# Kernel optimization log

Measured on AMD Instinct MI355X. Metric: run time of the kernel, lower is better.

Reference implementation:

```python
import jax, jax.numpy as jnp
import numpy as np
from jax import lax

PATCH = 3  # also hist_window since n_history = 1


def setup_inputs() -> dict:
    key = jax.random.key(0)
    k1, k2, k3 = jax.random.split(key, 3)
    B, Seq, F = 128, 3000, 64
    x = jax.random.normal(k1, (B, Seq, F), dtype=jnp.float32)
    agg_w = jax.random.normal(k2, (PATCH, PATCH), dtype=jnp.float32)  # Linear(hist_window=3 -> patch=3)
    agg_b = jax.random.normal(k3, (PATCH,), dtype=jnp.float32)
    return {"x": x, "agg_w": agg_w, "agg_b": agg_b}


def reference(x, agg_w, agg_b):
    # DDI forward with alpha=0.0 (default): for each patch i,
    #   prev   = output[:, i-patch:i, :]            (previous produced patch)
    #   agg    = gelu(Linear(prev.permute(0,2,1))).permute(0,2,1)
    #   output[:, i:i+patch, :] = agg + x[:, i:i+patch, :]
    # Dropout is identity (eval). Strict sequential dep -> lax.scan over chunks.
    B, Seq, F = x.shape
    head = x[:, :PATCH, :]  # first hist_window tokens copied through
    n_chunks = (Seq - PATCH) // PATCH  # 999
    # [n_chunks, B, patch, F]
    chunks = jnp.swapaxes(x[:, PATCH:, :].reshape(B, n_chunks, PATCH, F), 0, 1)

    def step(prev, cur):
        # prev, cur: [B, patch, F]
        # Linear over history axis: out[b,p,f] = sum_h prev[b,h,f] * W[p,h] + b[p]
        agg = jnp.einsum('bhf,ph->bpf', prev, agg_w) + agg_b[None, :, None]
        agg = jax.nn.gelu(agg, approximate=False)  # torch F.gelu default is exact
        res = agg + cur
        return res, res

    _, out_chunks = lax.scan(step, head, chunks)  # [n_chunks, B, patch, F]
    tail = jnp.swapaxes(out_chunks, 0, 1).reshape(B, Seq - PATCH, F)
    return jnp.concatenate([head, tail], axis=1)
```

## Files before the change

kernel.cpp:

```cpp
#include <hip/hip_runtime.h>
#include <math.h>

#define SEQ   3000
#define FDIM  64

#define PPWc  0.23164189f
#define B1f   0.127414796f
#define B2f   (-0.142248368f)
#define B3f   0.7107068705f
#define B4f   (-0.7265760135f)
#define B5f   0.5307027145f
#define NL2Ef (-0.72134752044448170368f)

#define DECL9(p) float p##0,p##1,p##2,p##3,p##4,p##5,p##6,p##7,p##8
#define TOUCH9(P) "+v"(P##0),"+v"(P##1),"+v"(P##2),"+v"(P##3),"+v"(P##4),     \
    "+v"(P##5),"+v"(P##6),"+v"(P##7),"+v"(P##8)

#define PF1S(dst, OFF) asm volatile(                                          \
    "global_load_dword %0, %1, %2 offset:" #OFF                               \
    : "=v"(dst) : "v"(voff), "s"(lbase) : "memory")

#define WAITVM(Nlit, P) do {                                                  \
    asm volatile("s_waitcnt vmcnt(" #Nlit ")" : TOUCH9(P) : : "memory");      \
    __builtin_amdgcn_sched_barrier(0);                                        \
} while (0)

#define ASMA() asm volatile(                                                  \
    "v_fma_f32 %[a], %[wa], %[s], %[q]\n\t"                                   \
    "v_mov_b32_dpp %[d1], %[s] quad_perm:[1,2,0,0] row_mask:0xf bank_mask:0xf\n\t" \
    "v_mov_b32_dpp %[d2], %[s] quad_perm:[2,0,1,1] row_mask:0xf bank_mask:0xf\n\t" \
    "v_fmac_f32 %[a], %[wb], %[d1]\n\t"                                       \
    "v_fmac_f32 %[a], %[wc], %[d2]\n\t"                                       \
    "v_mul_f32 %[u2], %[a], %[a]\n\t"                                         \
    "v_max_f32 %[rl], 0, %[a]\n\t"                                            \
    "v_fma_f32 %[dd], %[ppw], abs(%[a]), 1.0\n\t"                             \
    "v_mul_f32 %[m], %[u2], %[nl2e]\n\t"                                      \
    "v_rcp_f32 %[r], %[dd]\n\t"                                               \
    "v_exp_f32 %[e], %[m]"                                                    \
    : [a]"=&v"(a_), [d1]"=&v"(d1_), [d2]"=&v"(d2_), [u2]"=&v"(u2_),           \
      [dd]"=&v"(dd_), [m]"=&v"(m_), [r]"=&v"(r_), [e]"=&v"(e_), [rl]"=&v"(rl_)\
    : [s]"v"(s), [wa]"v"(wA), [wb]"v"(wB), [wc]"v"(wC), [q]"v"(q),            \
      [ppw]"v"(cPPW), [nl2e]"v"(cNL2E))

#define ASMB(U, OFF) asm volatile(                                            \
    "v_fma_f32 %[c01], %[b2], %[r], %[b1]\n\t"                                \
    "v_fma_f32 %[c23], %[b4], %[r], %[b3]\n\t"                                \
    "v_mul_f32 %[rr], %[r], %[r]\n\t"                                         \
    "v_mul_f32 %[z], -abs(%[a]), %[e]\n\t"                                    \
    "v_add_f32 %[rlu], %[rl], %[u]\n\t"                                       \
    "v_fma_f32 %[pp], %[c23], %[rr], %[c01]\n\t"                              \
    "v_mul_f32 %[r4], %[rr], %[rr]\n\t"                                       \
    "v_mul_f32 %[zr], %[z], %[r]\n\t"                                         \
    "v_fmac_f32 %[pp], %[b5], %[r4]\n\t"                                      \
    "v_fma_f32 %[s], %[pp], %[zr], %[rlu]\n\t"                                \
    "global_store_dword %[vo], %[s], %[ob] offset:" #OFF                      \
    : [s]"=&v"(s), [c01]"=&v"(c01_), [c23]"=&v"(c23_), [rr]"=&v"(rr_),        \
      [r4]"=&v"(r4_), [pp]"=&v"(pp_), [zr]"=&v"(zr_), [z]"=&v"(z_),           \
      [rlu]"=&v"(rlu_)                                                        \
    : [a]"v"(a_), [r]"v"(r_), [e]"v"(e_), [rl]"v"(rl_), [u]"v"(U),            \
      [b1]"v"(cB1), [b2]"v"(cB2), [b3]"v"(cB3), [b4]"v"(cB4), [b5]"v"(cB5),   \
      [vo]"v"(voff), [ob]"s"(obase)                                           \
    : "memory")

#define STEP_LD(U, LD, OFF)  do { ASMA(); PF1S(LD, OFF); ASMB(U, OFF); } while (0)
#define STEP_NOLD(U, OFF)    do { ASMA(); ASMB(U, OFF); } while (0)

#define GRP_LD(P, L) do {                                                     \
    STEP_LD(P##0, L##0, 0); STEP_LD(P##1, L##1, 768); STEP_LD(P##2, L##2, 1536);\
    lbase += 576; obase += 576;                                               \
    STEP_LD(P##3, L##3, 0); STEP_LD(P##4, L##4, 768); STEP_LD(P##5, L##5, 1536);\
    lbase += 576; obase += 576;                                               \
    STEP_LD(P##6, L##6, 0); STEP_LD(P##7, L##7, 768); STEP_LD(P##8, L##8, 1536);\
    lbase += 576; obase += 576;                                               \
} while (0)

#define GRP_NOLD(P) do {                                                      \
    STEP_NOLD(P##0, 0); STEP_NOLD(P##1, 768); STEP_NOLD(P##2, 1536);          \
    obase += 576;                                                             \
    STEP_NOLD(P##3, 0); STEP_NOLD(P##4, 768); STEP_NOLD(P##5, 1536);          \
    obase += 576;                                                             \
    STEP_NOLD(P##6, 0); STEP_NOLD(P##7, 768); STEP_NOLD(P##8, 1536);          \
    obase += 576;                                                             \
} while (0)

#define PF3B(Pa, Pb, Pc) do {                                                 \
    PF1S(Pa, 0); PF1S(Pb, 768); PF1S(Pc, 1536); lbase += 576;                 \
} while (0)
#define PF9B(P) do { PF3B(P##0,P##1,P##2); PF3B(P##3,P##4,P##5);              \
    PF3B(P##6,P##7,P##8); } while (0)

__global__ __launch_bounds__(64, 1) void scan_kernel(
    const float* __restrict__ x,
    const float* __restrict__ w,
    const float* __restrict__ bias,
    float* __restrict__ out)
{
    const int lane = threadIdx.x;
    const int g  = lane >> 2;
    const int pr = lane & 3;
    const int p  = pr < 3 ? pr : 2;

    const int B = blockIdx.x;
    const int xs = B & 7, h = (B >> 3) & 1, j = B >> 4;
    const int i = j * 8 + xs;
    const int b = i >> 1;
    const int fq = ((i & 1) << 1) | h;
    const int f = (fq << 4) + g;

    const int p1i = (p + 1) == 3 ? 0 : p + 1;
    const int p2i = (p + 2) >= 3 ? p - 1 : p + 2;
    float wA = w[p * 3 + p];
    float wB = w[p * 3 + p1i];
    float wC = w[p * 3 + p2i];
    float q  = bias[p];

    float cPPW = PPWc, cNL2E = NL2Ef;
    float cB1 = B1f, cB2 = B2f, cB3 = B3f, cB4 = B4f, cB5 = B5f;

    const int voff = p * 256 + f * 4;
    const float* lbase = x   + (size_t)b * (SEQ * FDIM) + 3 * FDIM;
    float*       obase = out + (size_t)b * (SEQ * FDIM) + 3 * FDIM;
    const float* hbase = x   + (size_t)b * (SEQ * FDIM);
    float*       ohead = out + (size_t)b * (SEQ * FDIM);

    float s = *(const float*)((const char*)hbase + voff);
    asm volatile("" : "+v"(s), "+v"(wA), "+v"(wB), "+v"(wC), "+v"(q),
                      "+v"(cPPW), "+v"(cNL2E), "+v"(cB1), "+v"(cB2),
                      "+v"(cB3), "+v"(cB4), "+v"(cB5));
    asm volatile("global_store_dword %0, %1, %2"
                 :: "v"(voff), "v"(s), "s"(ohead) : "memory");

    float a_, d1_, d2_, u2_, dd_, m_, r_, e_, rl_;
    float c01_, c23_, rr_, r4_, pp_, zr_, z_, rlu_;

    DECL9(LA); DECL9(LB); DECL9(LC); DECL9(LD);

    PF9B(LA);
    PF9B(LB);
    PF9B(LC);
    WAITVM(18, LA);

    #pragma unroll 1
    for (int t = 0; t < 27; ++t) {
        GRP_LD(LA, LD);   WAITVM(27, LB);
        GRP_LD(LB, LA);   WAITVM(27, LC);
        GRP_LD(LC, LB);   WAITVM(27, LD);
        GRP_LD(LD, LC);   WAITVM(27, LA);
    }

    GRP_NOLD(LA);         WAITVM(9, LB);
    GRP_NOLD(LB);         WAITVM(9, LC);
    GRP_NOLD(LC);
}

extern "C" void kernel_launch(void* const* d_in, const int* in_sizes, int n_in,
                              void* d_out, int out_size, void* d_ws, size_t ws_size,
                              hipStream_t stream) {
    const float* x    = (const float*)d_in[0];
    const float* w    = (const float*)d_in[1];
    const float* bias = (const float*)d_in[2];
    float* out        = (float*)d_out;

    hipLaunchKernelGGL(scan_kernel, dim3(512), dim3(64), 0, stream,
                       x, w, bias, out);
}
```

Measured before the change: 61.03 us.

## Process two feature columns per lane with interleaved dual recurrence chains

Each lane now carries two independent scan chains (adjacent features X and Y), interleaving their instructions so one chain's ALU/transcendental latency hides behind the other's. The grid halves from 512 to 256 single-wave blocks, with block-to-(batch,feature) mapping simplified. This adds ILP on the latency-bound serial recurrence at the cost of more registers, half as many wavefronts across the GPU, and a different memory access pattern per block.

Result: slower. 102.9 us (+68.7%).

```diff
diff --git a/kernel.cpp b/kernel.cpp
--- a/kernel.cpp
+++ b/kernel.cpp
@@ -16,78 +16,121 @@
 #define TOUCH9(P) "+v"(P##0),"+v"(P##1),"+v"(P##2),"+v"(P##3),"+v"(P##4),     \
     "+v"(P##5),"+v"(P##6),"+v"(P##7),"+v"(P##8)
 
-#define PF1S(dst, OFF) asm volatile(                                          \
-    "global_load_dword %0, %1, %2 offset:" #OFF                               \
-    : "=v"(dst) : "v"(voff), "s"(lbase) : "memory")
-
-#define WAITVM(Nlit, P) do {                                                  \
-    asm volatile("s_waitcnt vmcnt(" #Nlit ")" : TOUCH9(P) : : "memory");      \
+#define PF2S(dX, dY, OFF) asm volatile(                                       \
+    "global_load_dword %0, %2, %4 offset:" #OFF "\n\t"                        \
+    "global_load_dword %1, %3, %4 offset:" #OFF                               \
+    : "=v"(dX), "=v"(dY) : "v"(voffX), "v"(voffY), "s"(lbase) : "memory")
+
+#define ST2(OFF) asm volatile(                                                \
+    "global_store_dword %0, %2, %4 offset:" #OFF "\n\t"                       \
+    "global_store_dword %1, %3, %4 offset:" #OFF                              \
+    :: "v"(voffX), "v"(voffY), "v"(sx), "v"(sy), "s"(obase) : "memory")
+
+#define WAITVM2(Nlit, PX, PY) do {                                            \
+    asm volatile("s_waitcnt vmcnt(" #Nlit ")"                                 \
+                 : TOUCH9(PX), TOUCH9(PY) : : "memory");                      \
     __builtin_amdgcn_sched_barrier(0);                                        \
 } while (0)
 
-#define ASMA() asm volatile(                                                  \
-    "v_fma_f32 %[a], %[wa], %[s], %[q]\n\t"                                   \
-    "v_mov_b32_dpp %[d1], %[s] quad_perm:[1,2,0,0] row_mask:0xf bank_mask:0xf\n\t" \
-    "v_mov_b32_dpp %[d2], %[s] quad_perm:[2,0,1,1] row_mask:0xf bank_mask:0xf\n\t" \
-    "v_fmac_f32 %[a], %[wb], %[d1]\n\t"                                       \
-    "v_fmac_f32 %[a], %[wc], %[d2]\n\t"                                       \
-    "v_mul_f32 %[u2], %[a], %[a]\n\t"                                         \
-    "v_max_f32 %[rl], 0, %[a]\n\t"                                            \
-    "v_fma_f32 %[dd], %[ppw], abs(%[a]), 1.0\n\t"                             \
-    "v_mul_f32 %[m], %[u2], %[nl2e]\n\t"                                      \
-    "v_rcp_f32 %[r], %[dd]\n\t"                                               \
-    "v_exp_f32 %[e], %[m]"                                                    \
-    : [a]"=&v"(a_), [d1]"=&v"(d1_), [d2]"=&v"(d2_), [u2]"=&v"(u2_),           \
-      [dd]"=&v"(dd_), [m]"=&v"(m_), [r]"=&v"(r_), [e]"=&v"(e_), [rl]"=&v"(rl_)\
-    : [s]"v"(s), [wa]"v"(wA), [wb]"v"(wB), [wc]"v"(wC), [q]"v"(q),            \
-      [ppw]"v"(cPPW), [nl2e]"v"(cNL2E))
-
-#define ASMB(U, OFF) asm volatile(                                            \
-    "v_fma_f32 %[c01], %[b2], %[r], %[b1]\n\t"                                \
-    "v_fma_f32 %[c23], %[b4], %[r], %[b3]\n\t"                                \
-    "v_mul_f32 %[rr], %[r], %[r]\n\t"                                         \
-    "v_mul_f32 %[z], -abs(%[a]), %[e]\n\t"                                    \
-    "v_add_f32 %[rlu], %[rl], %[u]\n\t"                                       \
-    "v_fma_f32 %[pp], %[c23], %[rr], %[c01]\n\t"                              \
-    "v_mul_f32 %[r4], %[rr], %[rr]\n\t"                                       \
-    "v_mul_f32 %[zr], %[z], %[r]\n\t"                                         \
-    "v_fmac_f32 %[pp], %[b5], %[r4]\n\t"                                      \
-    "v_fma_f32 %[s], %[pp], %[zr], %[rlu]\n\t"                                \
-    "global_store_dword %[vo], %[s], %[ob] offset:" #OFF                      \
-    : [s]"=&v"(s), [c01]"=&v"(c01_), [c23]"=&v"(c23_), [rr]"=&v"(rr_),        \
-      [r4]"=&v"(r4_), [pp]"=&v"(pp_), [zr]"=&v"(zr_), [z]"=&v"(z_),           \
-      [rlu]"=&v"(rlu_)                                                        \
-    : [a]"v"(a_), [r]"v"(r_), [e]"v"(e_), [rl]"v"(rl_), [u]"v"(U),            \
-      [b1]"v"(cB1), [b2]"v"(cB2), [b3]"v"(cB3), [b4]"v"(cB4), [b5]"v"(cB5),   \
-      [vo]"v"(voff), [ob]"s"(obase)                                           \
-    : "memory")
-
-#define STEP_LD(U, LD, OFF)  do { ASMA(); PF1S(LD, OFF); ASMB(U, OFF); } while (0)
-#define STEP_NOLD(U, OFF)    do { ASMA(); ASMB(U, OFF); } while (0)
-
-#define GRP_LD(P, L) do {                                                     \
-    STEP_LD(P##0, L##0, 0); STEP_LD(P##1, L##1, 768); STEP_LD(P##2, L##2, 1536);\
+#define ASMA2() asm volatile(                                                 \
+    "v_fma_f32 %[aX], %[wa], %[sX], %[q]\n\t"                                 \
+    "v_fma_f32 %[aY], %[wa], %[sY], %[q]\n\t"                                 \
+    "v_mov_b32_dpp %[d1X], %[sX] quad_perm:[1,2,0,0] row_mask:0xf bank_mask:0xf\n\t" \
+    "v_mov_b32_dpp %[d1Y], %[sY] quad_perm:[1,2,0,0] row_mask:0xf bank_mask:0xf\n\t" \
+    "v_mov_b32_dpp %[d2X], %[sX] quad_perm:[2,0,1,1] row_mask:0xf bank_mask:0xf\n\t" \
+    "v_mov_b32_dpp %[d2Y], %[sY] quad_perm:[2,0,1,1] row_mask:0xf bank_mask:0xf\n\t" \
+    "v_fmac_f32 %[aX], %[wb], %[d1X]\n\t"                                     \
+    "v_fmac_f32 %[aY], %[wb], %[d1Y]\n\t"                                     \
+    "v_fmac_f32 %[aX], %[wc], %[d2X]\n\t"                                     \
+    "v_fmac_f32 %[aY], %[wc], %[d2Y]\n\t"                                     \
+    "v_mul_f32 %[u2X], %[aX], %[aX]\n\t"                                      \
+    "v_mul_f32 %[u2Y], %[aY], %[aY]\n\t"                                      \
+    "v_max_f32 %[rlX], 0, %[aX]\n\t"                                          \
+    "v_max_f32 %[rlY], 0, %[aY]\n\t"                                          \
+    "v_fma_f32 %[ddX], %[ppw], abs(%[aX]), 1.0\n\t"                           \
+    "v_fma_f32 %[ddY], %[ppw], abs(%[aY]), 1.0\n\t"                           \
+    "v_mul_f32 %[u2X], %[u2X], %[nl2e]\n\t"                                   \
+    "v_mul_f32 %[u2Y], %[u2Y], %[nl2e]\n\t"                                   \
+    "v_rcp_f32 %[rX], %[ddX]\n\t"                                             \
+    "v_rcp_f32 %[rY], %[ddY]\n\t"                                             \
+    "v_exp_f32 %[eX], %[u2X]\n\t"                                             \
+    "v_exp_f32 %[eY], %[u2Y]"                                                 \
+    : [aX]"=&v"(aX_), [d1X]"=&v"(d1X_), [d2X]"=&v"(d2X_), [u2X]"=&v"(u2X_),   \
+      [ddX]"=&v"(ddX_), [rX]"=&v"(rX_), [eX]"=&v"(eX_), [rlX]"=&v"(rlX_),     \
+      [aY]"=&v"(aY_), [d1Y]"=&v"(d1Y_), [d2Y]"=&v"(d2Y_), [u2Y]"=&v"(u2Y_),   \
+      [ddY]"=&v"(ddY_), [rY]"=&v"(rY_), [eY]"=&v"(eY_), [rlY]"=&v"(rlY_)      \
+    : [sX]"v"(sx), [sY]"v"(sy), [wa]"v"(wA), [wb]"v"(wB), [wc]"v"(wC),        \
+      [q]"v"(q), [ppw]"v"(cPPW), [nl2e]"v"(cNL2E))
+
+#define ASMB2(UX, UY) asm volatile(                                           \
+    "v_fma_f32 %[c01X], %[b2], %[rX], %[b1]\n\t"                              \
+    "v_fma_f32 %[c01Y], %[b2], %[rY], %[b1]\n\t"                              \
+    "v_fma_f32 %[c23X], %[b4], %[rX], %[b3]\n\t"                              \
+    "v_fma_f32 %[c23Y], %[b4], %[rY], %[b3]\n\t"                              \
+    "v_mul_f32 %[rrX], %[rX], %[rX]\n\t"                                      \
+    "v_mul_f32 %[rrY], %[rY], %[rY]\n\t"                                      \
+    "v_mul_f32 %[zX], -abs(%[aX]), %[eX]\n\t"                                 \
+    "v_mul_f32 %[zY], -abs(%[aY]), %[eY]\n\t"                                 \
+    "v_add_f32 %[rluX], %[rlX], %[uX]\n\t"                                    \
+    "v_add_f32 %[rluY], %[rlY], %[uY]\n\t"                                    \
+    "v_fma_f32 %[c23X], %[c23X], %[rrX], %[c01X]\n\t"                         \
+    "v_fma_f32 %[c23Y], %[c23Y], %[rrY], %[c01Y]\n\t"                         \
+    "v_mul_f32 %[r4X], %[rrX], %[rrX]\n\t"                                    \
+    "v_mul_f32 %[r4Y], %[rrY], %[rrY]\n\t"                                    \
+    "v_mul_f32 %[zX], %[zX], %[rX]\n\t"                                       \
+    "v_mul_f32 %[zY], %[zY], %[rY]\n\t"                                       \
+    "v_fmac_f32 %[c23X], %[b5], %[r4X]\n\t"                                   \
+    "v_fmac_f32 %[c23Y], %[b5], %[r4Y]\n\t"                                   \
+    "v_fma_f32 %[sX], %[c23X], %[zX], %[rluX]\n\t"                            \
+    "v_fma_f32 %[sY], %[c23Y], %[zY], %[rluY]"                                \
+    : [sX]"=&v"(sx), [c01X]"=&v"(c01X_), [c23X]"=&v"(c23X_),                  \
+      [rrX]"=&v"(rrX_), [r4X]"=&v"(r4X_), [zX]"=&v"(zX_), [rluX]"=&v"(rluX_), \
+      [sY]"=&v"(sy), [c01Y]"=&v"(c01Y_), [c23Y]"=&v"(c23Y_),                  \
+      [rrY]"=&v"(rrY_), [r4Y]"=&v"(r4Y_), [zY]"=&v"(zY_), [rluY]"=&v"(rluY_)  \
+    : [aX]"v"(aX_), [rX]"v"(rX_), [eX]"v"(eX_), [rlX]"v"(rlX_), [uX]"v"(UX),  \
+      [aY]"v"(aY_), [rY]"v"(rY_), [eY]"v"(eY_), [rlY]"v"(rlY_), [uY]"v"(UY),  \
+      [b1]"v"(cB1), [b2]"v"(cB2), [b3]"v"(cB3), [b4]"v"(cB4), [b5]"v"(cB5))
+
+#define STEPP_LD(UX, UY, LX, LY, OFF) do {                                    \
+    ASMA2(); PF2S(LX, LY, OFF); ASMB2(UX, UY); ST2(OFF); } while (0)
+#define STEPP_NOLD(UX, UY, OFF) do {                                          \
+    ASMA2(); ASMB2(UX, UY); ST2(OFF); } while (0)
+
+#define GRP_LD(PX, PY, LX, LY) do {                                           \
+    STEPP_LD(PX##0, PY##0, LX##0, LY##0, 0);                                  \
+    STEPP_LD(PX##1, PY##1, LX##1, LY##1, 768);                                \
+    STEPP_LD(PX##2, PY##2, LX##2, LY##2, 1536);                               \
     lbase += 576; obase += 576;                                               \
-    STEP_LD(P##3, L##3, 0); STEP_LD(P##4, L##4, 768); STEP_LD(P##5, L##5, 1536);\
+    STEPP_LD(PX##3, PY##3, LX##3, LY##3, 0);                                  \
+    STEPP_LD(PX##4, PY##4, LX##4, LY##4, 768);                                \
+    STEPP_LD(PX##5, PY##5, LX##5, LY##5, 1536);                               \
     lbase += 576; obase += 576;                                               \
-    STEP_LD(P##6, L##6, 0); STEP_LD(P##7, L##7, 768); STEP_LD(P##8, L##8, 1536);\
+    STEPP_LD(PX##6, PY##6, LX##6, LY##6, 0);                                  \
+    STEPP_LD(PX##7, PY##7, LX##7, LY##7, 768);                                \
+    STEPP_LD(PX##8, PY##8, LX##8, LY##8, 1536);                               \
     lbase += 576; obase += 576;                                               \
 } while (0)
 
-#define GRP_NOLD(P) do {                                                      \
-    STEP_NOLD(P##0, 0); STEP_NOLD(P##1, 768); STEP_NOLD(P##2, 1536);          \
-    obase += 576;                                                             \
-    STEP_NOLD(P##3, 0); STEP_NOLD(P##4, 768); STEP_NOLD(P##5, 1536);          \
-    obase += 576;                                                             \
-    STEP_NOLD(P##6, 0); STEP_NOLD(P##7, 768); STEP_NOLD(P##8, 1536);          \
-    obase += 576;                                                             \
-} while (0)
-
-#define PF3B(Pa, Pb, Pc) do {                                                 \
-    PF1S(Pa, 0); PF1S(Pb, 768); PF1S(Pc, 1536); lbase += 576;                 \
-} while (0)
-#define PF9B(P) do { PF3B(P##0,P##1,P##2); PF3B(P##3,P##4,P##5);              \
-    PF3B(P##6,P##7,P##8); } while (0)
+#define GRP_NOLD(PX, PY) do {                                                 \
+    STEPP_NOLD(PX##0, PY##0, 0);                                              \
+    STEPP_NOLD(PX##1, PY##1, 768);                                            \
+    STEPP_NOLD(PX##2, PY##2, 1536);  obase += 576;                            \
+    STEPP_NOLD(PX##3, PY##3, 0);                                              \
+    STEPP_NOLD(PX##4, PY##4, 768);                                            \
+    STEPP_NOLD(PX##5, PY##5, 1536);  obase += 576;                            \
+    STEPP_NOLD(PX##6, PY##6, 0);                                              \
+    STEPP_NOLD(PX##7, PY##7, 768);                                            \
+    STEPP_NOLD(PX##8, PY##8, 1536);  obase += 576;                            \
+} while (0)
+
+#define PF9B2(PX, PY) do {                                                    \
+    PF2S(PX##0, PY##0, 0); PF2S(PX##1, PY##1, 768);                           \
+    PF2S(PX##2, PY##2, 1536); lbase += 576;                                   \
+    PF2S(PX##3, PY##3, 0); PF2S(PX##4, PY##4, 768);                           \
+    PF2S(PX##5, PY##5, 1536); lbase += 576;                                   \
+    PF2S(PX##6, PY##6, 0); PF2S(PX##7, PY##7, 768);                           \
+    PF2S(PX##8, PY##8, 1536); lbase += 576;                                   \
+} while (0)
 
 __global__ __launch_bounds__(64, 1) void scan_kernel(
     const float* __restrict__ x,
@@ -100,12 +143,9 @@
     const int pr = lane & 3;
     const int p  = pr < 3 ? pr : 2;
 
-    const int B = blockIdx.x;
-    const int xs = B & 7, h = (B >> 3) & 1, j = B >> 4;
-    const int i = j * 8 + xs;
-    const int b = i >> 1;
-    const int fq = ((i & 1) << 1) | h;
-    const int f = (fq << 4) + g;
+    const int b = blockIdx.x >> 1;
+    const int h = blockIdx.x & 1;
+    const int j = h * 16 + g;
 
     const int p1i = (p + 1) == 3 ? 0 : p + 1;
     const int p2i = (p + 2) >= 3 ? p - 1 : p + 2;
@@ -117,40 +157,47 @@
     float cPPW = PPWc, cNL2E = NL2Ef;
     float cB1 = B1f, cB2 = B2f, cB3 = B3f, cB4 = B4f, cB5 = B5f;
 
-    const int voff = p * 256 + f * 4;
+    const int voffX = p * 256 + j * 8;
+    const int voffY = voffX + 4;
     const float* lbase = x   + (size_t)b * (SEQ * FDIM) + 3 * FDIM;
     float*       obase = out + (size_t)b * (SEQ * FDIM) + 3 * FDIM;
     const float* hbase = x   + (size_t)b * (SEQ * FDIM);
     float*       ohead = out + (size_t)b * (SEQ * FDIM);
 
-    float s = *(const float*)((const char*)hbase + voff);
-    asm volatile("" : "+v"(s), "+v"(wA), "+v"(wB), "+v"(wC), "+v"(q),
-                      "+v"(cPPW), "+v"(cNL2E), "+v"(cB1), "+v"(cB2),
+    float sx = *(const float*)((const char*)hbase + voffX);
+    float sy = *(const float*)((const char*)hbase + voffY);
+    asm volatile("" : "+v"(sx), "+v"(sy), "+v"(wA), "+v"(wB), "+v"(wC),
+                      "+v"(q), "+v"(cPPW), "+v"(cNL2E), "+v"(cB1), "+v"(cB2),
                       "+v"(cB3), "+v"(cB4), "+v"(cB5));
-    asm volatile("global_store_dword %0, %1, %2"
-                 :: "v"(voff), "v"(s), "s"(ohead) : "memory");
-
-    float a_, d1_, d2_, u2_, dd_, m_, r_, e_, rl_;
-    float c01_, c23_, rr_, r4_, pp_, zr_, z_, rlu_;
-
-    DECL9(LA); DECL9(LB); DECL9(LC); DECL9(LD);
-
-    PF9B(LA);
-    PF9B(LB);
-    PF9B(LC);
-    WAITVM(18, LA);
+    asm volatile("global_store_dword %0, %2, %4\n\t"
+                 "global_store_dword %1, %3, %4"
+                 :: "v"(voffX), "v"(voffY), "v"(sx), "v"(sy), "s"(ohead)
+                 : "memory");
+
+    float aX_, d1X_, d2X_, u2X_, ddX_, rX_, eX_, rlX_;
+    float aY_, d1Y_, d2Y_, u2Y_, ddY_, rY_, eY_, rlY_;
+    float c01X_, c23X_, rrX_, r4X_, zX_, rluX_;
+    float c01Y_, c23Y_, rrY_, r4Y_, zY_, rluY_;
+
+    DECL9(LAX); DECL9(LAY); DECL9(LBX); DECL9(LBY);
+    DECL9(LCX); DECL9(LCY); DECL9(LDX); DECL9(LDY);
+
+    PF9B2(LAX, LAY);
+    PF9B2(LBX, LBY);
+    PF9B2(LCX, LCY);
+    WAITVM2(36, LAX, LAY);
 
     #pragma unroll 1
     for (int t = 0; t < 27; ++t) {
-        GRP_LD(LA, LD);   WAITVM(27, LB);
-        GRP_LD(LB, LA);   WAITVM(27, LC);
-        GRP_LD(LC, LB);   WAITVM(27, LD);
-        GRP_LD(LD, LC);   WAITVM(27, LA);
+        GRP_LD(LAX, LAY, LDX, LDY);   WAITVM2(54, LBX, LBY);
+        GRP_LD(LBX, LBY, LAX, LAY);   WAITVM2(54, LCX, LCY);
+        GRP_LD(LCX, LCY, LBX, LBY);   WAITVM2(54, LDX, LDY);
+        GRP_LD(LDX, LDY, LCX, LCY);   WAITVM2(54, LAX, LAY);
     }
 
-    GRP_NOLD(LA);         WAITVM(9, LB);
-    GRP_NOLD(LB);         WAITVM(9, LC);
-    GRP_NOLD(LC);
+    GRP_NOLD(LAX, LAY);   WAITVM2(18, LBX, LBY);
+    GRP_NOLD(LBX, LBY);   WAITVM2(18, LCX, LCY);
+    GRP_NOLD(LCX, LCY);
 }
 
 extern "C" void kernel_launch(void* const* d_in, const int* in_sizes, int n_in,
@@ -161,6 +208,6 @@
     const float* bias = (const float*)d_in[2];
     float* out        = (float*)d_out;
 
-    hipLaunchKernelGGL(scan_kernel, dim3(512), dim3(64), 0, stream,
+    hipLaunchKernelGGL(scan_kernel, dim3(256), dim3(64), 0, stream,
                        x, w, bias, out);
 }
```
